# Optimization experiments

Hardware: AMD Instinct MI355X
Metric: run time of the kernel (lower is better)

## Reference

```python
import jax, jax.numpy as jnp
import numpy as np

B, T, NCH, NBIN, NBAND = 2, 400, 8, 512, 40
NPV = NCH * NCH


def setup_inputs() -> dict:
    key = jax.random.key(0)
    ks = jax.random.split(key, 7)
    bins_real = jax.random.normal(ks[0], (B, T, NCH, NBIN), jnp.float32)
    bins_imag = jax.random.normal(ks[1], (B, T, NCH, NBIN), jnp.float32)
    band_matrix_real = jax.random.normal(ks[2], (NBIN, NBAND), jnp.float32) * 0.05
    band_matrix_imag = jax.random.normal(ks[3], (NBIN, NBAND), jnp.float32) * 0.05
    cov_to_pv_real = jax.random.normal(ks[4], (NPV, NCH * NCH), jnp.float32) * 0.1
    cov_to_pv_imag = jax.random.normal(ks[5], (NPV, NCH * NCH), jnp.float32) * 0.1
    tau = jax.random.uniform(ks[6], (NBAND,), jnp.float32, 0.8, 0.99)
    return {
        'bins_real': bins_real, 'bins_imag': bins_imag,
        'band_matrix_real': band_matrix_real, 'band_matrix_imag': band_matrix_imag,
        'cov_to_pv_real': cov_to_pv_real, 'cov_to_pv_imag': cov_to_pv_imag,
        'tau': tau,
    }


def _power_vector(bins_real, bins_imag, band_matrix_real, band_matrix_imag,
                  cov_to_pv_real, cov_to_pv_imag, tau):
    x = jax.lax.complex(bins_real, bins_imag)            # (B,T,C,F)
    nch = x.shape[-2]
    EPS = 1e-20
    # per-bin covariance outer product, flattened cov dim: (B,T,F,C*C)
    cov = jnp.einsum('btif,btjf->btfij', x, jnp.conj(x))
    b, t, f = cov.shape[:3]
    cov = cov.reshape(b, t, f, nch * nch)
    diag = jnp.arange(nch) * (nch + 1)                   # diagonal indices in cov dim
    trace = jnp.clip(jnp.sum(cov.real[..., diag], axis=-1, keepdims=True), EPS, None)
    cov = cov / trace                                    # per-bin trace normalisation
    # phase adjustment along the bin axis (n=1 -> lag of 2 bins)
    c = jnp.swapaxes(cov, -1, -2)                        # (B,T,C2,F)
    prod = jnp.conj(c[..., :-2]) * c[..., 2:]
    ang = jnp.arctan2(prod.imag, prod.real)
    ang = jnp.concatenate([ang[..., :1], ang, ang[..., -1:]], axis=-1)  # edge pad
    adj = jnp.abs(c) * jax.lax.complex(jnp.cos(ang), jnp.sin(ang))
    adj = adj.at[..., diag, :].set(c[..., diag, :])      # keep original diagonals
    # band projection: contract bins against (F,K) band matrix
    bm = jax.lax.complex(band_matrix_real, band_matrix_imag)
    band_cov = jnp.einsum('btcf,fk->btkc', adj, bm)      # (B,T,K,C2)
    dsum = jnp.clip(band_cov.real[..., diag].sum(-1, keepdims=True), EPS, None)
    band_cov = band_cov / dsum
    # first-order IIR smoothing over frames, per-band pole tau
    a = tau[:, None].astype(band_cov.real.dtype)         # (K,1)
    def step(carry, xt):
        y = a * carry + (1.0 - a) * xt
        return y, y
    y0 = jnp.zeros_like(band_cov[:, 0])                  # (B,K,C2)
    _, ys = jax.lax.scan(step, y0, jnp.moveaxis(band_cov, 1, 0))
    band_cov = jnp.moveaxis(ys, 0, 1)                    # (B,T,K,C2)
    # cov -> power vector projection, real part
    c2p = jax.lax.complex(cov_to_pv_real, cov_to_pv_imag)  # (P,C2)
    pv = jnp.einsum('pc,btkc->btkp', c2p, band_cov).real   # (B,T,K,P)
    return pv


def reference(bins_real, bins_imag, band_matrix_real, band_matrix_imag,
              cov_to_pv_real, cov_to_pv_imag, tau):
    return _power_vector(bins_real, bins_imag, band_matrix_real, band_matrix_imag,
                         cov_to_pv_real, cov_to_pv_imag, tau)
```

## Files before the change

kernel.cpp:

```cpp
#include <hip/hip_runtime.h>
#include <hip/hip_fp16.h>

#define B_    2
#define T_    400
#define NCH_  8
#define NBIN_ 512
#define NBAND_ 40
#define NPV_  64

using half8   = __attribute__((ext_vector_type(8))) _Float16;
using float4v = __attribute__((ext_vector_type(4))) float;

static __device__ inline unsigned pkhf(float x, float y) {
  __half2 h = __float22half2_rn(make_float2(x, y));
  return __builtin_bit_cast(unsigned, h);
}
static __device__ inline unsigned rot16(unsigned u) {
  return (u >> 16) | (u << 16);
}
static __device__ inline unsigned cmulc(unsigned viu, unsigned vju) {
  __half2 Vi = __builtin_bit_cast(__half2, viu);
  __half2 Vj = __builtin_bit_cast(__half2, vju);
  __half2 P1 = __hmul2(Vi, __low2half2(Vj));
  __half2 Qi = __lowhigh2highlow(Vi);
  unsigned tn = __builtin_bit_cast(unsigned, __high2half2(Vj)) ^ 0x80000000u;
  __half2 a  = __hfma2(Qi, __builtin_bit_cast(__half2, tn), P1);
  return __builtin_bit_cast(unsigned, a);
}

__global__ __launch_bounds__(256) void pv_prep(
    const float* __restrict__ bmr, const float* __restrict__ bmi,
    const float* __restrict__ c2pr, const float* __restrict__ c2pi,
    float* __restrict__ ws)
{
  const int tid = threadIdx.x;
  const int blk = blockIdx.x;
  if (blk == 0) {
    __shared__ float sds[256];
    int k = tid & 63, part = tid >> 6;
    float s = 0.f;
    if (k < NBAND_) {
      const float* col = bmr + k;
      #pragma unroll 16
      for (int f = part * 128; f < part * 128 + 128; f++) s += col[f * 40];
    }
    sds[tid] = s;
    __syncthreads();
    if (tid < NBAND_) {
      float t = sds[tid] + sds[tid + 64] + sds[tid + 128] + sds[tid + 192];
      ws[tid] = 1.0f / fmaxf(t, 1e-20f);
    }
  } else if (blk <= 24) {
    int F = (blk - 1) * 256 + tid;
    int l = F & 63;
    int fid = F >> 6;
    int s5 = fid / 3;
    int n = fid - s5 * 3;
    int k = n * 16 + (l & 15);
    int quad = l >> 4;
    unsigned dw[4];
    #pragma unroll
    for (int t2 = 0; t2 < 4; t2++) {
      float v0 = 0.f, v1 = 0.f;
      if (k < NBAND_) {
        int f = s5 * 16 + quad * 4 + t2;
        v0 = bmr[f * 40 + k]; v1 = bmi[f * 40 + k];
      }
      dw[t2] = pkhf(v0, v1);
    }
    ((uint4*)((char*)ws + 1024))[F] = make_uint4(dw[0], dw[1], dw[2], dw[3]);
  } else {
    int F2 = (blk - 25) * 256 + tid;
    int lane = F2 & 63, E = F2 >> 6;
    int nt = E >> 2, ks = E & 3;
    int n = lane & 15, quad = lane >> 4;
    int p = nt * 16 + n;
    unsigned dw[4];
    #pragma unroll
    for (int t2 = 0; t2 < 4; t2++) {
      int c = ks * 16 + quad * 4 + t2;
      dw[t2] = pkhf(c2pr[p * 64 + c], -c2pi[p * 64 + c]);
    }
    ((uint4*)((char*)ws + 197632))[E * 64 + lane] = make_uint4(dw[0], dw[1], dw[2], dw[3]);
  }
}

__global__ __launch_bounds__(256, 3) void pv_main(
    const float* __restrict__ br, const float* __restrict__ bi,
    const float* __restrict__ ws, float* __restrict__ out)
{
  __shared__ __align__(16) unsigned smem[4096];

  const int bt  = blockIdx.x;
  const int tid = threadIdx.x;

  const int mt   = tid >> 6;
  const int lane = tid & 63;
  const int m16  = lane & 15;
  const int quad = lane >> 4;
  const int p    = mt * 16 + m16;
  const int ich  = p >> 3, jch = p & 7;
  const uint4* BF0 = (const uint4*)((const char*)ws + 1024);

  {
    const float* pr  = br + (size_t)bt * (NCH_ * NBIN_);
    const float* pim = bi + (size_t)bt * (NCH_ * NBIN_);
    unsigned* vsh = smem;
    const int f0 = 2 * tid;
    if (tid == 0 || tid == 255) {
      #pragma unroll
      for (int bb = 0; bb < 2; bb++) {
        const int f = f0 + bb;
        const int fm = (f == 0) ? 0 : ((f == 511) ? 509 : f - 1);
        const int fp = (f == 0) ? 2 : ((f == 511) ? 511 : f + 1);
        float tr = 0.f;
        float t1[8], t2[8];
        #pragma unroll
        for (int c = 0; c < 8; c++) {
          const float* cr = pr + c * 512;
          const float* ci = pim + c * 512;
          float xr = cr[f],   xi = ci[f];
          float xrm = cr[fm], xim = ci[fm];
          float xrp = cr[fp], xip = ci[fp];
          tr = fmaf(xr, xr, tr); tr = fmaf(xi, xi, tr);
          float Gr = fmaf(xrm, xrp,  xim * xip);
          float Gi = fmaf(xrm, xip, -(xim * xrp));
          float am = fmaxf(fmaxf(fabsf(Gr), fabsf(Gi)), 1e-30f);
          float rc = __builtin_amdgcn_rcpf(am);
          float q1 = Gr * rc, q2 = Gi * rc;
          float n2 = fmaf(q1, q1, q2 * q2);
          float rn = __builtin_amdgcn_rsqf(n2);
          bool ok = n2 > 0.f;
          float ur = ok ? q1 * rn : 1.f;
          float ui = ok ? q2 * rn : 0.f;
          float mg = __builtin_amdgcn_sqrtf(fmaf(xr, xr, xi * xi));
          t1[c] = mg * ur; t2[c] = mg * ui;
        }
        float scv = __builtin_amdgcn_rsqf(fmaxf(tr, 1e-20f));
        const int fc = f >> 2, fl = f & 3;
        #pragma unroll
        for (int c = 0; c < 8; c++)
          vsh[c * 512 + ((fc ^ c) << 2) + fl] = pkhf(t1[c] * scv, t2[c] * scv);
      }
    } else {
      const int base = f0 - 1;
      float tra = 0.f, trb = 0.f;
      float t1a[8], t2a[8], t1b[8], t2b[8];
      #pragma unroll
      for (int c = 0; c < 8; c++) {
        float4 wr, wi;
        __builtin_memcpy(&wr, pr + c * 512 + base, 16);
        __builtin_memcpy(&wi, pim + c * 512 + base, 16);
        {
          float xr = wr.y, xi = wi.y;
          float xrm = wr.x, xim = wi.x;
          float xrp = wr.z, xip = wi.z;
          tra = fmaf(xr, xr, tra); tra = fmaf(xi, xi, tra);
          float Gr = fmaf(xrm, xrp,  xim * xip);
          float Gi = fmaf(xrm, xip, -(xim * xrp));
          float am = fmaxf(fmaxf(fabsf(Gr), fabsf(Gi)), 1e-30f);
          float rc = __builtin_amdgcn_rcpf(am);
          float q1 = Gr * rc, q2 = Gi * rc;
          float n2 = fmaf(q1, q1, q2 * q2);
          float rn = __builtin_amdgcn_rsqf(n2);
          bool ok = n2 > 0.f;
          float ur = ok ? q1 * rn : 1.f;
          float ui = ok ? q2 * rn : 0.f;
          float mg = __builtin_amdgcn_sqrtf(fmaf(xr, xr, xi * xi));
          t1a[c] = mg * ur; t2a[c] = mg * ui;
        }
        {
          float xr = wr.z, xi = wi.z;
          float xrm = wr.y, xim = wi.y;
          float xrp = wr.w, xip = wi.w;
          trb = fmaf(xr, xr, trb); trb = fmaf(xi, xi, trb);
          float Gr = fmaf(xrm, xrp,  xim * xip);
          float Gi = fmaf(xrm, xip, -(xim * xrp));
          float am = fmaxf(fmaxf(fabsf(Gr), fabsf(Gi)), 1e-30f);
          float rc = __builtin_amdgcn_rcpf(am);
          float q1 = Gr * rc, q2 = Gi * rc;
          float n2 = fmaf(q1, q1, q2 * q2);
          float rn = __builtin_amdgcn_rsqf(n2);
          bool ok = n2 > 0.f;
          float ur = ok ? q1 * rn : 1.f;
          float ui = ok ? q2 * rn : 0.f;
          float mg = __builtin_amdgcn_sqrtf(fmaf(xr, xr, xi * xi));
          t1b[c] = mg * ur; t2b[c] = mg * ui;
        }
      }
      float scva = __builtin_amdgcn_rsqf(fmaxf(tra, 1e-20f));
      float scvb = __builtin_amdgcn_rsqf(fmaxf(trb, 1e-20f));
      const int fc = f0 >> 2, fl = f0 & 3;
      #pragma unroll
      for (int c = 0; c < 8; c++) {
        unsigned d0 = pkhf(t1a[c] * scva, t2a[c] * scva);
        unsigned d1 = pkhf(t1b[c] * scvb, t2b[c] * scvb);
        *(uint2*)(vsh + c * 512 + ((fc ^ c) << 2) + fl) = make_uint2(d0, d1);
      }
    }
  }
  __syncthreads();

  float4v acc[6];
  #pragma unroll
  for (int g = 0; g < 6; g++) acc[g] = (float4v){0.f, 0.f, 0.f, 0.f};

  const uint4* Bg = BF0 + lane;
  uint4 pa0 = Bg[0],   pa1 = Bg[64],  pa2 = Bg[128];
  uint4 pb0 = Bg[192], pb1 = Bg[256], pb2 = Bg[320];
  #pragma unroll 4
  for (int s = 0; s < 32; s++) {
    uint4 cb0 = pa0, cb1 = pa1, cb2 = pa2;
    pa0 = pb0; pa1 = pb1; pa2 = pb2;
    {
      const uint4* nx = Bg + (size_t)(((s + 2) & 31) * 192);
      pb0 = nx[0]; pb1 = nx[64]; pb2 = nx[128];
    }
    const int sc = s * 4 + quad;
    half8 b0 = __builtin_bit_cast(half8, cb0);
    half8 b1 = __builtin_bit_cast(half8, cb1);
    half8 b2 = __builtin_bit_cast(half8, cb2);
    const uint4* vb = (const uint4*)smem;
    uint4 av = vb[ich * 128 + (sc ^ ich)];
    uint4 bv = vb[jch * 128 + (sc ^ jch)];
    unsigned a0 = cmulc(av.x, bv.x);
    unsigned a1 = cmulc(av.y, bv.y);
    unsigned a2 = cmulc(av.z, bv.z);
    unsigned a3 = cmulc(av.w, bv.w);
    uint4 au1 = make_uint4(a0 ^ 0x80000000u, a1 ^ 0x80000000u,
                           a2 ^ 0x80000000u, a3 ^ 0x80000000u);
    uint4 au2 = make_uint4(rot16(a0), rot16(a1),
                           rot16(a2), rot16(a3));
    half8 af1 = __builtin_bit_cast(half8, au1);
    half8 af2 = __builtin_bit_cast(half8, au2);
    acc[0] = __builtin_amdgcn_mfma_f32_16x16x32_f16(af1, b0, acc[0], 0, 0, 0);
    acc[3] = __builtin_amdgcn_mfma_f32_16x16x32_f16(af2, b0, acc[3], 0, 0, 0);
    acc[1] = __builtin_amdgcn_mfma_f32_16x16x32_f16(af1, b1, acc[1], 0, 0, 0);
    acc[4] = __builtin_amdgcn_mfma_f32_16x16x32_f16(af2, b1, acc[4], 0, 0, 0);
    acc[2] = __builtin_amdgcn_mfma_f32_16x16x32_f16(af1, b2, acc[2], 0, 0, 0);
    acc[5] = __builtin_amdgcn_mfma_f32_16x16x32_f16(af2, b2, acc[5], 0, 0, 0);
  }
  __syncthreads();

  const uint4* EF = ((const uint4*)((const char*)ws + 197632)) + (mt * 4) * 64 + lane;
  uint4 eb[4];
  #pragma unroll
  for (int ks = 0; ks < 4; ks++) eb[ks] = EF[ks * 64];

  {
    unsigned* bcsh = smem;
    #pragma unroll
    for (int n = 0; n < 3; n++) {
      uint4 w4 = make_uint4(pkhf(acc[n][0], acc[n+3][0]),
                            pkhf(acc[n][1], acc[n+3][1]),
                            pkhf(acc[n][2], acc[n+3][2]),
                            pkhf(acc[n][3], acc[n+3][3]));
      *(uint4*)(bcsh + (n * 16 + m16) * 68 + mt * 16 + quad * 4) = w4;
    }
  }
  __syncthreads();

  const float4* wsd = (const float4*)ws;
  {
    const unsigned* bcsh = smem;
    float4v eacc[3];
    #pragma unroll
    for (int kt = 0; kt < 3; kt++) eacc[kt] = (float4v){0.f, 0.f, 0.f, 0.f};
    #pragma unroll
    for (int ks = 0; ks < 4; ks++) {
      half8 bfr = __builtin_bit_cast(half8, eb[ks]);
      #pragma unroll
      for (int kt = 0; kt < 3; kt++) {
        uint4 a4 = *(const uint4*)(bcsh + (kt * 16 + m16) * 68 + ks * 16 + quad * 4);
        half8 afr = __builtin_bit_cast(half8, a4);
        eacc[kt] = __builtin_amdgcn_mfma_f32_16x16x32_f16(afr, bfr, eacc[kt], 0, 0, 0);
      }
    }
    float* op = out + (size_t)bt * (NBAND_ * NPV_);
    #pragma unroll
    for (int kt = 0; kt < 3; kt++) {
      float4 dv = wsd[kt * 4 + quad];
      float dva[4] = {dv.x, dv.y, dv.z, dv.w};
      #pragma unroll
      for (int r = 0; r < 4; r++) {
        int k = kt * 16 + quad * 4 + r;
        if (k < NBAND_)
          op[k * 64 + mt * 16 + m16] = eacc[kt][r] * dva[r];
      }
    }
  }
}

__global__ __launch_bounds__(640) void pv_iir4(float* __restrict__ z,
                                               const float* __restrict__ tau)
{
  __shared__ float gsh[40][16];
  const int pg = blockIdx.x & 3;
  const int bk = blockIdx.x >> 2;
  const int k = bk % NBAND_;
  const int b = bk / NBAND_;
  const float a  = tau[k];
  const float om = 1.0f - a;
  const int c  = threadIdx.x >> 4;
  const int pl = threadIdx.x & 15;
  const int p  = pg * 16 + pl;
  const size_t stride = (size_t)NBAND_ * 64;
  size_t idx0 = (size_t)b * (T_ * NBAND_ * 64) + (size_t)(c * 10) * stride + k * 64 + p;

  float y[10];
  float accv = 0.f;
  #pragma unroll
  for (int i = 0; i < 10; i++) {
    float v = z[idx0 + (size_t)i * stride];
    accv = fmaf(a, accv, om * v);
    y[i] = accv;
  }
  gsh[c][pl] = accv;
  __syncthreads();
  float a2 = a * a, a4 = a2 * a2, a8 = a4 * a4;
  float A = a8 * a2;
  float H = 0.f;
  #pragma unroll
  for (int d = 0; d < 39; d++) {
    float g = gsh[d][pl];
    H = (d < c) ? fmaf(A, H, g) : H;
  }
  float wp = a;
  #pragma unroll
  for (int i = 0; i < 10; i++) {
    z[idx0 + (size_t)i * stride] = fmaf(wp, H, y[i]);
    wp *= a;
  }
}

extern "C" void kernel_launch(void* const* d_in, const int* in_sizes, int n_in,
                              void* d_out, int out_size, void* d_ws, size_t ws_size,
                              hipStream_t stream)
{
  const float* br   = (const float*)d_in[0];
  const float* bi   = (const float*)d_in[1];
  const float* bmr  = (const float*)d_in[2];
  const float* bmi  = (const float*)d_in[3];
  const float* c2pr = (const float*)d_in[4];
  const float* c2pi = (const float*)d_in[5];
  const float* tau  = (const float*)d_in[6];
  float* out = (float*)d_out;
  float* ws  = (float*)d_ws;

  hipLaunchKernelGGL(pv_prep, dim3(29), dim3(256), 0, stream,
                     bmr, bmi, c2pr, c2pi, ws);
  hipLaunchKernelGGL(pv_main, dim3(B_ * T_), dim3(256), 0, stream,
                     br, bi, ws, out);
  hipLaunchKernelGGL(pv_iir4, dim3(B_ * NBAND_ * 4), dim3(640), 0, stream,
                     out, tau);
}
```

Measured before the change: 112.3 us.

## Split main kernel into global-staged phase prep and band-split GEMM grid

The per-frame phase-adjust stage moves into the prep kernel and writes packed half-precision adjusted covariance inputs to global workspace instead of shared memory. A new GEMM kernel runs on a 2D grid (frame × band tile of 16), so each block computes one band tile with fewer accumulators and lower register and LDS pressure, which allows more blocks in flight. The cost is a global round trip of 16KB per frame, recomputation of the complex outer products three times (once per band tile), and an extra kernel boundary.

```diff
diff --git a/kernel.cpp b/kernel.cpp
--- a/kernel.cpp
+++ b/kernel.cpp
@@ -7,6 +7,7 @@
 #define NBIN_ 512
 #define NBAND_ 40
 #define NPV_  64
+#define A_OFF (1u << 20)
 
 using half8   = __attribute__((ext_vector_type(8))) _Float16;
 using float4v = __attribute__((ext_vector_type(4))) float;
@@ -28,9 +29,10 @@
   return __builtin_bit_cast(unsigned, a);
 }
 
-__global__ __launch_bounds__(256) void pv_prep(
+__global__ __launch_bounds__(256, 3) void pv_prep(
     const float* __restrict__ bmr, const float* __restrict__ bmi,
     const float* __restrict__ c2pr, const float* __restrict__ c2pi,
+    const float* __restrict__ br, const float* __restrict__ bi,
     float* __restrict__ ws)
 {
   const int tid = threadIdx.x;
@@ -69,7 +71,7 @@
       dw[t2] = pkhf(v0, v1);
     }
     ((uint4*)((char*)ws + 1024))[F] = make_uint4(dw[0], dw[1], dw[2], dw[3]);
-  } else {
+  } else if (blk <= 28) {
     int F2 = (blk - 25) * 256 + tid;
     int lane = F2 & 63, E = F2 >> 6;
     int nt = E >> 2, ks = E & 3;
@@ -82,30 +84,11 @@
       dw[t2] = pkhf(c2pr[p * 64 + c], -c2pi[p * 64 + c]);
     }
     ((uint4*)((char*)ws + 197632))[E * 64 + lane] = make_uint4(dw[0], dw[1], dw[2], dw[3]);
-  }
-}
-
-__global__ __launch_bounds__(256, 3) void pv_main(
-    const float* __restrict__ br, const float* __restrict__ bi,
-    const float* __restrict__ ws, float* __restrict__ out)
-{
-  __shared__ __align__(16) unsigned smem[4096];
-
-  const int bt  = blockIdx.x;
-  const int tid = threadIdx.x;
-
-  const int mt   = tid >> 6;
-  const int lane = tid & 63;
-  const int m16  = lane & 15;
-  const int quad = lane >> 4;
-  const int p    = mt * 16 + m16;
-  const int ich  = p >> 3, jch = p & 7;
-  const uint4* BF0 = (const uint4*)((const char*)ws + 1024);
-
-  {
+  } else {
+    const int bt = blk - 29;
     const float* pr  = br + (size_t)bt * (NCH_ * NBIN_);
     const float* pim = bi + (size_t)bt * (NCH_ * NBIN_);
-    unsigned* vsh = smem;
+    unsigned* vg = (unsigned*)((char*)ws + A_OFF) + (size_t)bt * 4096;
     const int f0 = 2 * tid;
     if (tid == 0 || tid == 255) {
       #pragma unroll
@@ -140,7 +123,7 @@
         const int fc = f >> 2, fl = f & 3;
         #pragma unroll
         for (int c = 0; c < 8; c++)
-          vsh[c * 512 + ((fc ^ c) << 2) + fl] = pkhf(t1[c] * scv, t2[c] * scv);
+          vg[c * 512 + ((fc ^ c) << 2) + fl] = pkhf(t1[c] * scv, t2[c] * scv);
       }
     } else {
       const int base = f0 - 1;
@@ -195,34 +178,52 @@
       for (int c = 0; c < 8; c++) {
         unsigned d0 = pkhf(t1a[c] * scva, t2a[c] * scva);
         unsigned d1 = pkhf(t1b[c] * scvb, t2b[c] * scvb);
-        *(uint2*)(vsh + c * 512 + ((fc ^ c) << 2) + fl) = make_uint2(d0, d1);
+        *(uint2*)(vg + c * 512 + ((fc ^ c) << 2) + fl) = make_uint2(d0, d1);
       }
     }
   }
-  __syncthreads();
-
-  float4v acc[6];
-  #pragma unroll
-  for (int g = 0; g < 6; g++) acc[g] = (float4v){0.f, 0.f, 0.f, 0.f};
-
-  const uint4* Bg = BF0 + lane;
-  uint4 pa0 = Bg[0],   pa1 = Bg[64],  pa2 = Bg[128];
-  uint4 pb0 = Bg[192], pb1 = Bg[256], pb2 = Bg[320];
+}
+
+__global__ __launch_bounds__(256, 4) void pv_gemm(
+    const float* __restrict__ ws, float* __restrict__ out)
+{
+  __shared__ __align__(16) unsigned bcsh[16 * 68];
+
+  const int bt = blockIdx.x;
+  const int n  = blockIdx.y;
+  const int tid = threadIdx.x;
+  const int mt   = tid >> 6;
+  const int lane = tid & 63;
+  const int m16  = lane & 15;
+  const int quad = lane >> 4;
+  const int p    = mt * 16 + m16;
+  const int ich  = p >> 3, jch = p & 7;
+
+  const uint4* AF  = (const uint4*)((const char*)ws + A_OFF) + (size_t)bt * 1024;
+  const uint4* Bg  = (const uint4*)((const char*)ws + 1024) + n * 64 + lane;
+
+  float4v acc[2];
+  acc[0] = (float4v){0.f, 0.f, 0.f, 0.f};
+  acc[1] = (float4v){0.f, 0.f, 0.f, 0.f};
+
+  uint4 b_0 = Bg[0];
+  uint4 b_1 = Bg[192];
+  int sc0 = quad, sc1 = 4 + quad;
+  uint4 av0 = AF[ich * 128 + (sc0 ^ ich)], bv0 = AF[jch * 128 + (sc0 ^ jch)];
+  uint4 av1 = AF[ich * 128 + (sc1 ^ ich)], bv1 = AF[jch * 128 + (sc1 ^ jch)];
+
   #pragma unroll 4
   for (int s = 0; s < 32; s++) {
-    uint4 cb0 = pa0, cb1 = pa1, cb2 = pa2;
-    pa0 = pb0; pa1 = pb1; pa2 = pb2;
+    uint4 cb = b_0, av = av0, bv = bv0;
+    b_0 = b_1; av0 = av1; bv0 = bv1;
     {
-      const uint4* nx = Bg + (size_t)(((s + 2) & 31) * 192);
-      pb0 = nx[0]; pb1 = nx[64]; pb2 = nx[128];
-    }
-    const int sc = s * 4 + quad;
-    half8 b0 = __builtin_bit_cast(half8, cb0);
-    half8 b1 = __builtin_bit_cast(half8, cb1);
-    half8 b2 = __builtin_bit_cast(half8, cb2);
-    const uint4* vb = (const uint4*)smem;
-    uint4 av = vb[ich * 128 + (sc ^ ich)];
-    uint4 bv = vb[jch * 128 + (sc ^ jch)];
+      const int s2 = (s + 2) & 31;
+      const int sc2 = s2 * 4 + quad;
+      b_1 = Bg[(size_t)s2 * 192];
+      av1 = AF[ich * 128 + (sc2 ^ ich)];
+      bv1 = AF[jch * 128 + (sc2 ^ jch)];
+    }
+    half8 b0 = __builtin_bit_cast(half8, cb);
     unsigned a0 = cmulc(av.x, bv.x);
     unsigned a1 = cmulc(av.y, bv.y);
     unsigned a2 = cmulc(av.z, bv.z);
@@ -234,13 +235,8 @@
     half8 af1 = __builtin_bit_cast(half8, au1);
     half8 af2 = __builtin_bit_cast(half8, au2);
     acc[0] = __builtin_amdgcn_mfma_f32_16x16x32_f16(af1, b0, acc[0], 0, 0, 0);
-    acc[3] = __builtin_amdgcn_mfma_f32_16x16x32_f16(af2, b0, acc[3], 0, 0, 0);
-    acc[1] = __builtin_amdgcn_mfma_f32_16x16x32_f16(af1, b1, acc[1], 0, 0, 0);
-    acc[4] = __builtin_amdgcn_mfma_f32_16x16x32_f16(af2, b1, acc[4], 0, 0, 0);
-    acc[2] = __builtin_amdgcn_mfma_f32_16x16x32_f16(af1, b2, acc[2], 0, 0, 0);
-    acc[5] = __builtin_amdgcn_mfma_f32_16x16x32_f16(af2, b2, acc[5], 0, 0, 0);
-  }
-  __syncthreads();
+    acc[1] = __builtin_amdgcn_mfma_f32_16x16x32_f16(af2, b0, acc[1], 0, 0, 0);
+  }
 
   const uint4* EF = ((const uint4*)((const char*)ws + 197632)) + (mt * 4) * 64 + lane;
   uint4 eb[4];
@@ -248,45 +244,32 @@
   for (int ks = 0; ks < 4; ks++) eb[ks] = EF[ks * 64];
 
   {
-    unsigned* bcsh = smem;
-    #pragma unroll
-    for (int n = 0; n < 3; n++) {
-      uint4 w4 = make_uint4(pkhf(acc[n][0], acc[n+3][0]),
-                            pkhf(acc[n][1], acc[n+3][1]),
-                            pkhf(acc[n][2], acc[n+3][2]),
-                            pkhf(acc[n][3], acc[n+3][3]));
-      *(uint4*)(bcsh + (n * 16 + m16) * 68 + mt * 16 + quad * 4) = w4;
-    }
+    uint4 w4 = make_uint4(pkhf(acc[0][0], acc[1][0]),
+                          pkhf(acc[0][1], acc[1][1]),
+                          pkhf(acc[0][2], acc[1][2]),
+                          pkhf(acc[0][3], acc[1][3]));
+    *(uint4*)(bcsh + m16 * 68 + mt * 16 + quad * 4) = w4;
   }
   __syncthreads();
 
-  const float4* wsd = (const float4*)ws;
   {
-    const unsigned* bcsh = smem;
-    float4v eacc[3];
-    #pragma unroll
-    for (int kt = 0; kt < 3; kt++) eacc[kt] = (float4v){0.f, 0.f, 0.f, 0.f};
+    float4v eacc = (float4v){0.f, 0.f, 0.f, 0.f};
     #pragma unroll
     for (int ks = 0; ks < 4; ks++) {
       half8 bfr = __builtin_bit_cast(half8, eb[ks]);
-      #pragma unroll
-      for (int kt = 0; kt < 3; kt++) {
-        uint4 a4 = *(const uint4*)(bcsh + (kt * 16 + m16) * 68 + ks * 16 + quad * 4);
-        half8 afr = __builtin_bit_cast(half8, a4);
-        eacc[kt] = __builtin_amdgcn_mfma_f32_16x16x32_f16(afr, bfr, eacc[kt], 0, 0, 0);
-      }
-    }
+      uint4 a4 = *(const uint4*)(bcsh + m16 * 68 + ks * 16 + quad * 4);
+      half8 afr = __builtin_bit_cast(half8, a4);
+      eacc = __builtin_amdgcn_mfma_f32_16x16x32_f16(afr, bfr, eacc, 0, 0, 0);
+    }
+    const float4* wsd = (const float4*)ws;
+    float4 dv = wsd[n * 4 + quad];
+    float dva[4] = {dv.x, dv.y, dv.z, dv.w};
     float* op = out + (size_t)bt * (NBAND_ * NPV_);
     #pragma unroll
-    for (int kt = 0; kt < 3; kt++) {
-      float4 dv = wsd[kt * 4 + quad];
-      float dva[4] = {dv.x, dv.y, dv.z, dv.w};
-      #pragma unroll
-      for (int r = 0; r < 4; r++) {
-        int k = kt * 16 + quad * 4 + r;
-        if (k < NBAND_)
-          op[k * 64 + mt * 16 + m16] = eacc[kt][r] * dva[r];
-      }
+    for (int r = 0; r < 4; r++) {
+      int k = n * 16 + quad * 4 + r;
+      if (k < NBAND_)
+        op[k * 64 + mt * 16 + m16] = eacc[r] * dva[r];
     }
   }
 }
@@ -347,10 +330,10 @@
   float* out = (float*)d_out;
   float* ws  = (float*)d_ws;
 
-  hipLaunchKernelGGL(pv_prep, dim3(29), dim3(256), 0, stream,
-                     bmr, bmi, c2pr, c2pi, ws);
-  hipLaunchKernelGGL(pv_main, dim3(B_ * T_), dim3(256), 0, stream,
-                     br, bi, ws, out);
+  hipLaunchKernelGGL(pv_prep, dim3(29 + B_ * T_), dim3(256), 0, stream,
+                     bmr, bmi, c2pr, c2pi, br, bi, ws);
+  hipLaunchKernelGGL(pv_gemm, dim3(B_ * T_, 3), dim3(256), 0, stream,
+                     ws, out);
   hipLaunchKernelGGL(pv_iir4, dim3(B_ * NBAND_ * 4), dim3(640), 0, stream,
                      out, tau);
 }
```

Measured after the change: 129.5 us. +15.3%, slower.

## Fuse weight-prep kernel into main kernel with flag-based inter-block sync

Applied to the files above, without the earlier changes.

Folds the small weight-packing kernel into the main kernel as its first 29 blocks. Each prep block publishes a per-block flag with a release store, and main blocks poll those flags with acquire loads and sleeps. Main blocks wait only after loading their inputs, phase-adjusting them and writing them to shared memory, just before the matrix loop that reads the packed weights. This removes one kernel launch boundary and lets the prep work overlap the front of the main work. The minimum occupancy hint also goes from 3 to 4 blocks. The flags are never reset, so later calls see them already set and may read weights while they are being rewritten. That is harmless only while the weights stay the same, and the higher occupancy target may cost register spills.

```diff
diff --git a/kernel.cpp b/kernel.cpp
--- a/kernel.cpp
+++ b/kernel.cpp
@@ -7,6 +7,8 @@
 #define NBIN_ 512
 #define NBAND_ 40
 #define NPV_  64
+#define NPREP_ 29
+#define MAGIC_ 0x13579BDFu
 
 using half8   = __attribute__((ext_vector_type(8))) _Float16;
 using float4v = __attribute__((ext_vector_type(4))) float;
@@ -28,71 +30,76 @@
   return __builtin_bit_cast(unsigned, a);
 }
 
-__global__ __launch_bounds__(256) void pv_prep(
+__global__ __launch_bounds__(256, 4) void pv_main(
     const float* __restrict__ bmr, const float* __restrict__ bmi,
     const float* __restrict__ c2pr, const float* __restrict__ c2pi,
-    float* __restrict__ ws)
+    const float* __restrict__ br, const float* __restrict__ bi,
+    float* __restrict__ ws, float* __restrict__ out)
 {
+  __shared__ __align__(16) unsigned smem[4096];
   const int tid = threadIdx.x;
   const int blk = blockIdx.x;
-  if (blk == 0) {
-    __shared__ float sds[256];
-    int k = tid & 63, part = tid >> 6;
-    float s = 0.f;
-    if (k < NBAND_) {
-      const float* col = bmr + k;
-      #pragma unroll 16
-      for (int f = part * 128; f < part * 128 + 128; f++) s += col[f * 40];
-    }
-    sds[tid] = s;
+  unsigned* flags = (unsigned*)ws + 128;
+
+  if (blk < NPREP_) {
+    if (blk == 0) {
+      __shared__ float sds[256];
+      int k = tid & 63, part = tid >> 6;
+      float s = 0.f;
+      if (k < NBAND_) {
+        const float* col = bmr + k;
+        #pragma unroll 16
+        for (int f = part * 128; f < part * 128 + 128; f++) s += col[f * 40];
+      }
+      sds[tid] = s;
+      __syncthreads();
+      if (tid < NBAND_) {
+        float t = sds[tid] + sds[tid + 64] + sds[tid + 128] + sds[tid + 192];
+        ws[tid] = 1.0f / fmaxf(t, 1e-20f);
+      }
+    } else if (blk <= 24) {
+      int F = (blk - 1) * 256 + tid;
+      int l = F & 63;
+      int fid = F >> 6;
+      int s5 = fid / 3;
+      int n = fid - s5 * 3;
+      int k = n * 16 + (l & 15);
+      int quad = l >> 4;
+      unsigned dw[4];
+      #pragma unroll
+      for (int t2 = 0; t2 < 4; t2++) {
+        float v0 = 0.f, v1 = 0.f;
+        if (k < NBAND_) {
+          int f = s5 * 16 + quad * 4 + t2;
+          v0 = bmr[f * 40 + k]; v1 = bmi[f * 40 + k];
+        }
+        dw[t2] = pkhf(v0, v1);
+      }
+      ((uint4*)((char*)ws + 1024))[F] = make_uint4(dw[0], dw[1], dw[2], dw[3]);
+    } else {
+      int F2 = (blk - 25) * 256 + tid;
+      int lane = F2 & 63, E = F2 >> 6;
+      int nt = E >> 2, ks = E & 3;
+      int n = lane & 15, quad = lane >> 4;
+      int p = nt * 16 + n;
+      unsigned dw[4];
+      #pragma unroll
+      for (int t2 = 0; t2 < 4; t2++) {
+        int c = ks * 16 + quad * 4 + t2;
+        dw[t2] = pkhf(c2pr[p * 64 + c], -c2pi[p * 64 + c]);
+      }
+      ((uint4*)((char*)ws + 197632))[E * 64 + lane] = make_uint4(dw[0], dw[1], dw[2], dw[3]);
+    }
     __syncthreads();
-    if (tid < NBAND_) {
-      float t = sds[tid] + sds[tid + 64] + sds[tid + 128] + sds[tid + 192];
-      ws[tid] = 1.0f / fmaxf(t, 1e-20f);
-    }
-  } else if (blk <= 24) {
-    int F = (blk - 1) * 256 + tid;
-    int l = F & 63;
-    int fid = F >> 6;
-    int s5 = fid / 3;
-    int n = fid - s5 * 3;
-    int k = n * 16 + (l & 15);
-    int quad = l >> 4;
-    unsigned dw[4];
-    #pragma unroll
-    for (int t2 = 0; t2 < 4; t2++) {
-      float v0 = 0.f, v1 = 0.f;
-      if (k < NBAND_) {
-        int f = s5 * 16 + quad * 4 + t2;
-        v0 = bmr[f * 40 + k]; v1 = bmi[f * 40 + k];
-      }
-      dw[t2] = pkhf(v0, v1);
-    }
-    ((uint4*)((char*)ws + 1024))[F] = make_uint4(dw[0], dw[1], dw[2], dw[3]);
-  } else {
-    int F2 = (blk - 25) * 256 + tid;
-    int lane = F2 & 63, E = F2 >> 6;
-    int nt = E >> 2, ks = E & 3;
-    int n = lane & 15, quad = lane >> 4;
-    int p = nt * 16 + n;
-    unsigned dw[4];
-    #pragma unroll
-    for (int t2 = 0; t2 < 4; t2++) {
-      int c = ks * 16 + quad * 4 + t2;
-      dw[t2] = pkhf(c2pr[p * 64 + c], -c2pi[p * 64 + c]);
-    }
-    ((uint4*)((char*)ws + 197632))[E * 64 + lane] = make_uint4(dw[0], dw[1], dw[2], dw[3]);
-  }
-}
-
-__global__ __launch_bounds__(256, 3) void pv_main(
-    const float* __restrict__ br, const float* __restrict__ bi,
-    const float* __restrict__ ws, float* __restrict__ out)
-{
-  __shared__ __align__(16) unsigned smem[4096];
-
-  const int bt  = blockIdx.x;
-  const int tid = threadIdx.x;
+    if (tid == 0) {
+      __threadfence();
+      __hip_atomic_store(&flags[blk], MAGIC_, __ATOMIC_RELEASE,
+                         __HIP_MEMORY_SCOPE_AGENT);
+    }
+    return;
+  }
+
+  const int bt  = blk - NPREP_;
 
   const int mt   = tid >> 6;
   const int lane = tid & 63;
@@ -201,6 +208,13 @@
   }
   __syncthreads();
 
+  if (tid < NPREP_) {
+    while (__hip_atomic_load(&flags[tid], __ATOMIC_ACQUIRE,
+                             __HIP_MEMORY_SCOPE_AGENT) != MAGIC_)
+      __builtin_amdgcn_s_sleep(2);
+  }
+  __syncthreads();
+
   float4v acc[6];
   #pragma unroll
   for (int g = 0; g < 6; g++) acc[g] = (float4v){0.f, 0.f, 0.f, 0.f};
@@ -347,10 +361,8 @@
   float* out = (float*)d_out;
   float* ws  = (float*)d_ws;
 
-  hipLaunchKernelGGL(pv_prep, dim3(29), dim3(256), 0, stream,
-                     bmr, bmi, c2pr, c2pi, ws);
-  hipLaunchKernelGGL(pv_main, dim3(B_ * T_), dim3(256), 0, stream,
-                     br, bi, ws, out);
+  hipLaunchKernelGGL(pv_main, dim3(NPREP_ + B_ * T_), dim3(256), 0, stream,
+                     bmr, bmi, c2pr, c2pi, br, bi, ws, out);
   hipLaunchKernelGGL(pv_iir4, dim3(B_ * NBAND_ * 4), dim3(640), 0, stream,
                      out, tau);
 }
```

Measured after the change: 124.5 us. 10.8% more time.
